# Kernel tuning notes

Measured on AMD Instinct MI355X. Metric: run time of the kernel, lower is better.

The kernel has to match this reference:

```python
import jax, jax.numpy as jnp
import numpy as np

B, H, W, DIM, NH = 4, 32, 32, 768, 12
HD = DIM // NH  # head_dim = 64


def setup_inputs() -> dict:
    key = jax.random.key(0)
    ks = jax.random.split(key, 12)
    n = lambda i, shape, s=1.0: jax.random.normal(ks[i], shape, jnp.float32) * s
    return {
        "q": n(0, (B, H, W, DIM)),
        "k": n(1, (B, H, W, DIM)),
        "v": n(2, (B, H, W, DIM)),
        # Linear weights stored as (in, out) so y = x @ W + b (equivalent to torch x @ W.T)
        "Wq": n(3, (DIM, DIM), 0.02), "bq": jnp.zeros((DIM,), jnp.float32),
        "Wk": n(4, (DIM, DIM), 0.02), "bk": jnp.zeros((DIM,), jnp.float32),
        "Wv": n(5, (DIM, DIM), 0.02), "bv": jnp.zeros((DIM,), jnp.float32),
        "Wp": n(6, (DIM, DIM), 0.02), "bp": jnp.zeros((DIM,), jnp.float32),
        # decomposed relative position tables: (2*size - 1, head_dim)
        "rel_pos_h": n(7, (2 * H - 1, HD), 0.02),
        "rel_pos_w": n(8, (2 * W - 1, HD), 0.02),
    }


def reference(q, k, v, Wq, bq, Wk, bk, Wv, bv, Wp, bp, rel_pos_h, rel_pos_w):
    scale = HD ** -0.5

    def to_heads(x, Wt, b):
        y = x.reshape(B, H * W, DIM) @ Wt + b          # (B, HW, DIM)
        return y.reshape(B, H * W, NH, HD).transpose(0, 2, 1, 3).reshape(B * NH, H * W, HD)

    qh = to_heads(q, Wq, bq)   # (B*NH, HW, HD)
    kh = to_heads(k, Wk, bk)
    vh = to_heads(v, Wv, bv)

    # scaled dot-product scores
    attn = jnp.einsum('bqd,bkd->bqk', qh * scale, kh)  # (B*NH, HW, HW)

    # decomposed relative position bias (q_size == k_size == input_size, no interpolation)
    idx_h = jnp.arange(H)[:, None] - jnp.arange(H)[None, :] + (H - 1)
    idx_w = jnp.arange(W)[:, None] - jnp.arange(W)[None, :] + (W - 1)
    Rh = rel_pos_h[idx_h]  # (H, H, HD)
    Rw = rel_pos_w[idx_w]  # (W, W, HD)
    rq = qh.reshape(B * NH, H, W, HD)  # unscaled q, as in torch add_decomposed_rel_pos
    rel_h = jnp.einsum('bhwc,hkc->bhwk', rq, Rh)  # (B*NH, H, W, H)
    rel_w = jnp.einsum('bhwc,wkc->bhwk', rq, Rw)  # (B*NH, H, W, W)

    attn = (attn.reshape(B * NH, H, W, H, W)
            + rel_h[:, :, :, :, None]
            + rel_w[:, :, :, None, :]).reshape(B * NH, H * W, H * W)

    attn = jax.nn.softmax(attn, axis=-1)
    x = (attn @ vh).reshape(B, NH, H, W, HD).transpose(0, 2, 3, 1, 4).reshape(B, H, W, DIM)
    return x @ Wp + bp
```

## Files before the change

kernel.cpp:

```cpp
#include <hip/hip_runtime.h>
#include <math.h>

#define DIM  768
#define NH   12
#define HD   64
#define HWN  1024
#define MROWS 4096

typedef __attribute__((ext_vector_type(8))) short short8;
typedef __attribute__((ext_vector_type(4))) float f32x4;
typedef _Float16 h8 __attribute__((ext_vector_type(8)));
typedef _Float16 h2 __attribute__((ext_vector_type(2)));

__device__ __forceinline__ void gl_lds16(const void* g, void* l) {
    __builtin_amdgcn_global_load_lds(
        (const __attribute__((address_space(1))) void*)g,
        (__attribute__((address_space(3))) void*)l, 16, 0, 0);
}

__global__ __launch_bounds__(256) void prep_kernel(
    const float* __restrict__ q, const float* __restrict__ k,
    const float* __restrict__ v,
    const float* __restrict__ Wq, const float* __restrict__ Wk,
    const float* __restrict__ Wv, const float* __restrict__ Wp,
    const float* __restrict__ rph, const float* __restrict__ rpw,
    _Float16* __restrict__ WtAll, _Float16* __restrict__ relTg,
    _Float16* __restrict__ xf16)
{
    __shared__ float Ws[64][65];
    const int b = blockIdx.x;
    const int t = threadIdx.x;

    if (b < 576) {
        const int z = b / 144, rem = b - z * 144;
        const int ky = rem / 12, nx = rem - ky * 12;
        const float* W = (z == 0) ? Wq : (z == 1) ? Wk : (z == 2) ? Wv : Wp;
        _Float16* Wt = WtAll + (size_t)z * 589824;
        const int k0 = ky * 64, n0 = nx * 64;
        {
            int r = t >> 2, c4 = (t & 3) * 16;
            #pragma unroll
            for (int u = 0; u < 16; u += 4)
                *(float4*)&Ws[r][c4 + u] = *(const float4*)(W + (size_t)(k0 + r) * DIM + n0 + c4 + u);
        }
        __syncthreads();
        const int n = t >> 2, kseg = (t & 3) * 16;
        h8 h0, h1;
        #pragma unroll
        for (int j = 0; j < 8; ++j) {
            h0[j] = (_Float16)Ws[kseg + j][n];
            h1[j] = (_Float16)Ws[kseg + 8 + j][n];
        }
        size_t base = (size_t)(n0 + n) * DIM + k0 + kseg;
        *(h8*)(Wt + base) = h0;
        *(h8*)(Wt + base + 8) = h1;
    } else if (b == 576) {
        const int row = t >> 1, c0 = (t & 1) * 32;
        const float* src = (row < 63) ? rph + (size_t)row * HD
                         : (row >= 64 && row < 127) ? rpw + (size_t)(row - 64) * HD
                         : nullptr;
        #pragma unroll
        for (int g = 0; g < 4; ++g) {
            h8 o;
            #pragma unroll
            for (int j = 0; j < 8; ++j)
                o[j] = src ? (_Float16)src[c0 + g * 8 + j] : (_Float16)0.0f;
            *(h8*)(relTg + (size_t)row * HD + c0 + g * 8) = o;
        }
    } else {
        const int N8 = MROWS * DIM / 8;
        int i = (b - 577) * 256 + t;
        const int stride = (gridDim.x - 577) * 256;
        for (; i < 3 * N8; i += stride) {
            const int sel = i / N8, j = i - sel * N8;
            const float* src = (sel == 0) ? q : (sel == 1) ? k : v;
            float4 a0 = ((const float4*)src)[j * 2];
            float4 a1 = ((const float4*)src)[j * 2 + 1];
            h8 o = {(_Float16)a0.x, (_Float16)a0.y, (_Float16)a0.z, (_Float16)a0.w,
                    (_Float16)a1.x, (_Float16)a1.y, (_Float16)a1.z, (_Float16)a1.w};
            *(h8*)(xf16 + (size_t)sel * (MROWS * DIM) + (size_t)j * 8) = o;
        }
    }
}

template<int AMODE>
__global__ __launch_bounds__(256, 3) void gemm_mfma_kernel(
    const _Float16* __restrict__ X0, const _Float16* __restrict__ WtAll,
    const float* __restrict__ bias0, const float* __restrict__ bias1,
    const float* __restrict__ bias2,
    void* __restrict__ Y0, void* __restrict__ Y1, void* __restrict__ Y2)
{
    constexpr int MT = (AMODE == 0) ? 128 : 64;
    constexpr int RF = MT / 32;
    __shared__ __align__(16) char smem[MT * 128 + 12 * 1024];
    constexpr int BOFF = MT * 128;

    const int t = threadIdx.x;
    const int w = t >> 6, lane = t & 63;
    const int l15 = lane & 15, l4 = lane >> 4;

    int sel, rb, cb;
    if (AMODE == 0) {
        const int sw = (blockIdx.x & 7) * 96 + (blockIdx.x >> 3);
        sel = sw >> 8;
        const int rem = sw & 255;
        rb = rem >> 3; cb = rem & 7;
    } else {
        const int sw = (blockIdx.x & 7) * 64 + (blockIdx.x >> 3);
        sel = 3;
        rb = sw >> 3; cb = sw & 7;
    }
    const int row0 = rb * MT, col0 = cb * 96;

    const char* Ab = (const char*)(X0 + (AMODE == 0 ? (size_t)sel * (MROWS * DIM) : 0));
    const _Float16* Bt = WtAll + (size_t)sel * 589824;
    const float* bias = (AMODE == 1) ? bias0 : (sel == 0) ? bias0 : (sel == 1) ? bias1 : bias2;

    f32x4 acc[RF][3];
    #pragma unroll
    for (int i = 0; i < RF; ++i)
        #pragma unroll
        for (int j = 0; j < 3; ++j) acc[i][j] = (f32x4){0, 0, 0, 0};

    for (int kt = 0; kt < 12; ++kt) {
        #pragma unroll
        for (int i = 0; i < MT / 32; ++i) {
            const int fi = w * (MT / 32) + i;
            const int row = fi * 8 + (lane >> 3);
            const int srcb = ((lane & 7) * 16) ^ ((row & 7) << 4);
            gl_lds16(Ab + (size_t)(row0 + row) * 1536 + kt * 128 + srcb, smem + fi * 1024);
        }
        #pragma unroll
        for (int it = 0; it < 3; ++it) {
            const int f = it * 4 + w;
            const int ks = f / 6, cf = f % 6;
            const size_t off = (size_t)(col0 + cf * 16 + l15) * 1536 + kt * 128 + ks * 64 + l4 * 16;
            gl_lds16((const char*)Bt + off, smem + BOFF + f * 1024);
        }
        __syncthreads();

        __builtin_amdgcn_s_setprio(1);
        #pragma unroll
        for (int ks = 0; ks < 2; ++ks) {
            h8 b[3];
            #pragma unroll
            for (int cf4 = 0; cf4 < 3; ++cf4) {
                const int fb = ks * 6 + (w & 1) * 3 + cf4;
                b[cf4] = *(const h8*)(smem + BOFF + fb * 1024 + lane * 16);
            }
            #pragma unroll
            for (int rf = 0; rf < RF; ++rf) {
                const int arow = (w >> 1) * (MT / 2) + rf * 16 + l15;
                const int base = arow * 128 + ((ks * 64 + l4 * 16) ^ ((arow & 7) << 4));
                h8 ah = *(const h8*)(smem + base);
                #pragma unroll
                for (int cf4 = 0; cf4 < 3; ++cf4)
                    acc[rf][cf4] = __builtin_amdgcn_mfma_f32_16x16x32_f16(ah, b[cf4], acc[rf][cf4], 0, 0, 0);
            }
        }
        __builtin_amdgcn_s_setprio(0);
        __syncthreads();
    }

    const int wrow0 = row0 + (w >> 1) * (MT / 2);
    const int wcol0 = col0 + (w & 1) * 48;
    #pragma unroll
    for (int cf4 = 0; cf4 < 3; ++cf4) {
        const int c = wcol0 + cf4 * 16 + l15;
        const float bb = bias[c];
        #pragma unroll
        for (int rf = 0; rf < RF; ++rf) {
            #pragma unroll
            for (int reg = 0; reg < 4; ++reg) {
                const int r = wrow0 + rf * 16 + l4 * 4 + reg;
                float y = acc[rf][cf4][reg] + bb;
                if (AMODE == 1) {
                    ((float*)Y0)[(size_t)r * DIM + c] = y;
                } else {
                    _Float16* Yh = (_Float16*)((sel == 0) ? Y0 : (sel == 1) ? Y1 : Y2);
                    size_t base = ((size_t)((r >> 10) * NH + (c >> 6)) * HWN + (r & 1023)) * HD + (c & 63);
                    Yh[base] = (_Float16)y;
                }
            }
        }
    }
}

#define AT_REL   0
#define AT_VT    8704
#define AT_P     25088
#define AT_KB    33280
#define AT_QF    8704
#define AT_RELT  17920
#define AT_PG    17920
#define AT_OF    8704
#define AT_TOTAL 49664

__global__ __launch_bounds__(256, 3) void attn_kernel(
    const _Float16* __restrict__ qh, const _Float16* __restrict__ kh,
    const _Float16* __restrict__ vh, const _Float16* __restrict__ relTg,
    _Float16* __restrict__ aout)
{
    __shared__ __align__(16) char smem[AT_TOTAL];
    const int bid = blockIdx.x;
    const int j   = bid >> 3;
    const int bh  = (bid & 7) * 6 + (j >> 4);
    const int qb  = j & 15;
    const int t  = threadIdx.x;
    const int w  = t >> 6;
    const int lane = t & 63;
    const int l15 = lane & 15, l4 = lane >> 4;

    _Float16* Rel = (_Float16*)(smem + AT_REL);
    _Float16* Qf  = (_Float16*)(smem + AT_QF);

    const int r = t >> 2, dc = (t & 3) * 16;
    {
        const _Float16* qp = qh + ((size_t)bh * HWN + qb * 64 + r) * HD + dc;
        *(short8*)(&Qf[r * 72 + dc])     = *(const short8*)(qp);
        *(short8*)(&Qf[r * 72 + dc + 8]) = *(const short8*)(qp + 8);
        #pragma unroll
        for (int it = 0; it < 4; ++it) {
            const int f = it * 4 + w;
            const int ct = f >> 1, ks = f & 1;
            gl_lds16((const char*)relTg + (ct * 16 + l15) * 128 + ks * 64 + l4 * 16,
                     smem + AT_RELT + f * 1024);
        }
    }
    __syncthreads();

    const _Float16* kb_ = kh + (size_t)bh * HWN * HD;
    const _Float16* vb_ = vh + (size_t)bh * HWN * HD;
    const int key2 = (t & 31) * 2, dgrp = t >> 5;
    short8 rv0, rv1;
#define LOADV(KT) {                                                            \
        const _Float16* vp = vb_ + (size_t)((KT) * 64 + key2) * HD + dgrp * 8; \
        rv0 = *(const short8*)vp; rv1 = *(const short8*)(vp + HD); }
    LOADV(0);

    h8 qf2[2];
    {
        const int qr = w * 16 + l15;
        qf2[0] = *(const h8*)(&Qf[qr * 72 + l4 * 8]);
        qf2[1] = *(const h8*)(&Qf[qr * 72 + 32 + l4 * 8]);
        #pragma unroll
        for (int j2 = 0; j2 < 8; ++j2) { qf2[0][j2] *= (_Float16)0.125f; qf2[1][j2] *= (_Float16)0.125f; }
    }

    f32x4 pacc[4][2];
    #pragma unroll
    for (int i = 0; i < 4; ++i)
        #pragma unroll
        for (int j2 = 0; j2 < 2; ++j2) pacc[i][j2] = (f32x4){0, 0, 0, 0};
    #pragma unroll
    for (int ks = 0; ks < 2; ++ks) {
        h8 b0 = *(const h8*)(smem + AT_RELT + ((w * 2 + 0) * 2 + ks) * 1024 + lane * 16);
        h8 b1 = *(const h8*)(smem + AT_RELT + ((w * 2 + 1) * 2 + ks) * 1024 + lane * 16);
        #pragma unroll
        for (int rt = 0; rt < 4; ++rt) {
            h8 a = *(const h8*)(&Qf[(rt * 16 + l15) * 72 + ks * 32 + l4 * 8]);
            pacc[rt][0] = __builtin_amdgcn_mfma_f32_16x16x32_f16(a, b0, pacc[rt][0], 0, 0, 0);
            pacc[rt][1] = __builtin_amdgcn_mfma_f32_16x16x32_f16(a, b1, pacc[rt][1], 0, 0, 0);
        }
    }

    __syncthreads();
    _Float16* Pg = (_Float16*)(smem + AT_PG);
    #pragma unroll
    for (int rt = 0; rt < 4; ++rt)
        #pragma unroll
        for (int cb2 = 0; cb2 < 2; ++cb2)
            #pragma unroll
            for (int reg = 0; reg < 4; ++reg)
                Pg[(rt * 16 + l4 * 4 + reg) * 130 + w * 32 + cb2 * 16 + l15] =
                    (_Float16)pacc[rt][cb2][reg];
    __syncthreads();

    {
        const int q = t >> 2, kk0 = (t & 3) * 8;
        const int hw = qb * 64 + q;
        const int hq = hw >> 5, wq = hw & 31;
        short8 vh_, vw_;
        #pragma unroll
        for (int j2 = 0; j2 < 8; ++j2) {
            const int kk = kk0 + j2;
            vh_[j2] = *(const short*)&Pg[q * 130 + (hq + 31 - kk)];
            vw_[j2] = *(const short*)&Pg[q * 130 + 64 + (wq + 31 - kk)];
        }
        *(short8*)(&Rel[q * 68 + kk0])      = vh_;
        *(short8*)(&Rel[q * 68 + 32 + kk0]) = vw_;
    }
    __syncthreads();

    const int qrow_bias = w * 16 + l15;
    float rw_[2][4];
    #pragma unroll
    for (int c2 = 0; c2 < 2; ++c2)
        #pragma unroll
        for (int reg = 0; reg < 4; ++reg)
            rw_[c2][reg] = (float)Rel[qrow_bias * 68 + 32 + c2 * 16 + l4 * 4 + reg];

#define STAGEK(KT, BUF) {                                                      \
        _Pragma("unroll")                                                      \
        for (int i2 = 0; i2 < 2; ++i2) {                                       \
            const int f = w * 2 + i2;                                          \
            const int keyk = f * 8 + (lane >> 3);                              \
            const int srcb = ((lane & 7) * 16) ^ ((lane >> 3) << 4);           \
            gl_lds16((const char*)kb_ + (size_t)((KT) * 64 + keyk) * 128 + srcb, \
                     smem + AT_KB + (BUF) * 8192 + f * 1024);                  \
        } }

#define WRITEVT(BUF) {                                                         \
        _Pragma("unroll")                                                      \
        for (int j2 = 0; j2 < 8; ++j2) {                                       \
            const int d = dgrp * 8 + j2;                                       \
            unsigned pk = ((unsigned short)rv0[j2]) |                          \
                          (((unsigned)(unsigned short)rv1[j2]) << 16);         \
            *(unsigned*)(smem + AT_VT + (BUF) * 8192 + d * 128 +               \
                         ((key2 * 2) ^ ((d & 7) << 4))) = pk; } }
    WRITEVT(0);
    STAGEK(0, 0);

    f32x4 acc_o[4] = {{0,0,0,0},{0,0,0,0},{0,0,0,0},{0,0,0,0}};
    float m_ = -INFINITY, lsum = 0.f;
    char* Pw = smem + AT_P + w * 2048;
    const int swzP = (l15 & 7) << 4;

    #pragma unroll 2
    for (int kt = 0; kt < 16; ++kt) {
        const int cur = kt & 1;
        __syncthreads();
        if (kt < 15) { LOADV(kt + 1); STAGEK(kt + 1, cur ^ 1); }

        h2 rhp = *(const h2*)(&Rel[qrow_bias * 68 + kt * 2]);
        const float rh0 = (float)rhp[0];
        const float rh1 = (float)rhp[1];
        f32x4 accs[4];
        #pragma unroll
        for (int ct = 0; ct < 4; ++ct) {
            const float rhc = (ct >> 1) ? rh1 : rh0;
            #pragma unroll
            for (int reg = 0; reg < 4; ++reg)
                accs[ct][reg] = rw_[ct & 1][reg] + rhc;
        }
        __builtin_amdgcn_s_setprio(1);
        #pragma unroll
        for (int ct = 0; ct < 4; ++ct) {
            const int row = ct * 16 + l15;
            const int swzK = (row & 7) << 4;
            #pragma unroll
            for (int ks = 0; ks < 2; ++ks) {
                h8 kfr = *(const h8*)(smem + AT_KB + cur * 8192 + row * 128 +
                                      ((ks * 64 + l4 * 16) ^ swzK));
                accs[ct] = __builtin_amdgcn_mfma_f32_16x16x32_f16(kfr, qf2[ks], accs[ct], 0, 0, 0);
            }
        }
        __builtin_amdgcn_s_setprio(0);

        float mx[4];
        #pragma unroll
        for (int ct = 0; ct < 4; ++ct)
            mx[ct] = fmaxf(fmaxf(accs[ct][0], accs[ct][1]),
                           fmaxf(accs[ct][2], accs[ct][3]));
        float tmax = fmaxf(fmaxf(mx[0], mx[1]), fmaxf(mx[2], mx[3]));

        if (__any(tmax > m_ + 8.f)) {
            float tg = fmaxf(tmax, __shfl_xor(tmax, 16));
            tg = fmaxf(tg, __shfl_xor(tg, 32));
            const float mnew = fmaxf(m_, tg);
            const float factor = __expf(m_ - mnew);
            m_ = mnew;
            lsum *= factor;
            #pragma unroll
            for (int reg = 0; reg < 4; ++reg) {
                const float fr = __shfl(factor, l4 * 4 + reg);
                #pragma unroll
                for (int dt = 0; dt < 4; ++dt) acc_o[dt][reg] *= fr;
            }
        }

        float tsum = 0.f;
        #pragma unroll
        for (int ct = 0; ct < 4; ++ct) {
            float p0 = __expf(accs[ct][0] - m_);
            float p1 = __expf(accs[ct][1] - m_);
            float p2 = __expf(accs[ct][2] - m_);
            float p3 = __expf(accs[ct][3] - m_);
            tsum += (p0 + p1) + (p2 + p3);
            h2 pa = {(_Float16)p0, (_Float16)p1};
            h2 pb = {(_Float16)p2, (_Float16)p3};
            uint2 pk;
            pk.x = *(unsigned*)&pa;
            pk.y = *(unsigned*)&pb;
            *(uint2*)(Pw + l15 * 128 + ((ct * 32 + l4 * 8) ^ swzP)) = pk;
        }
        lsum += tsum;

        __builtin_amdgcn_s_setprio(1);
        #pragma unroll
        for (int ks = 0; ks < 2; ++ks) {
            h8 pa = *(const h8*)(Pw + l15 * 128 + ((ks * 64 + l4 * 16) ^ swzP));
            #pragma unroll
            for (int dt = 0; dt < 4; ++dt) {
                const int d = dt * 16 + l15;
                h8 vf = *(const h8*)(smem + AT_VT + cur * 8192 + d * 128 +
                                     ((ks * 64 + l4 * 16) ^ ((d & 7) << 4)));
                acc_o[dt] = __builtin_amdgcn_mfma_f32_16x16x32_f16(pa, vf, acc_o[dt], 0, 0, 0);
            }
        }
        __builtin_amdgcn_s_setprio(0);

        if (kt < 15) WRITEVT(cur ^ 1);
    }

    float ltot = lsum + __shfl_xor(lsum, 16);
    ltot += __shfl_xor(ltot, 32);
    const float invl = 1.0f / ltot;
    float linv[4];
    #pragma unroll
    for (int reg = 0; reg < 4; ++reg) linv[reg] = __shfl(invl, l4 * 4 + reg);
    __syncthreads();
    _Float16* Of = (_Float16*)(smem + AT_OF);
    #pragma unroll
    for (int reg = 0; reg < 4; ++reg) {
        const int qloc = w * 16 + l4 * 4 + reg;
        #pragma unroll
        for (int dt = 0; dt < 4; ++dt)
            Of[qloc * 72 + dt * 16 + l15] = (_Float16)(acc_o[dt][reg] * linv[reg]);
    }
    __syncthreads();
    {
        const int b_ = bh / NH, nh = bh % NH;
        _Float16* op = aout + ((size_t)b_ * HWN + qb * 64 + r) * DIM + nh * HD + dc;
        *(short8*)op       = *(const short8*)(&Of[r * 72 + dc]);
        *(short8*)(op + 8) = *(const short8*)(&Of[r * 72 + dc + 8]);
    }
}

extern "C" void kernel_launch(void* const* d_in, const int* in_sizes, int n_in,
                              void* d_out, int out_size, void* d_ws, size_t ws_size,
                              hipStream_t stream) {
    const float* q   = (const float*)d_in[0];
    const float* k   = (const float*)d_in[1];
    const float* v   = (const float*)d_in[2];
    const float* Wq  = (const float*)d_in[3];
    const float* bq  = (const float*)d_in[4];
    const float* Wk  = (const float*)d_in[5];
    const float* bk  = (const float*)d_in[6];
    const float* Wv  = (const float*)d_in[7];
    const float* bv  = (const float*)d_in[8];
    const float* Wp  = (const float*)d_in[9];
    const float* bp  = (const float*)d_in[10];
    const float* rph = (const float*)d_in[11];
    const float* rpw = (const float*)d_in[12];

    float* out = (float*)d_out;
    char*  w0  = (char*)d_ws;

    _Float16* wtAll = (_Float16*)(w0);
    _Float16* relTg = (_Float16*)(w0 + 4718592);
    _Float16* xf16  = (_Float16*)(w0 + 4734976);
    _Float16* aout  = (_Float16*)(w0 + 4734976);
    _Float16* qf16  = (_Float16*)(w0 + 23609344);
    _Float16* kf16  = (_Float16*)(w0 + 29900800);
    _Float16* vf16  = (_Float16*)(w0 + 36192256);

    dim3 blk(256);
    prep_kernel<<<2625, blk, 0, stream>>>(q, k, v, Wq, Wk, Wv, Wp, rph, rpw,
                                          wtAll, relTg, xf16);
    gemm_mfma_kernel<0><<<768, blk, 0, stream>>>(
        xf16, wtAll, bq, bk, bv, qf16, kf16, vf16);
    attn_kernel<<<768, blk, 0, stream>>>(qf16, kf16, vf16, relTg, aout);
    gemm_mfma_kernel<1><<<512, blk, 0, stream>>>(
        aout, wtAll, bp, nullptr, nullptr, out, nullptr, nullptr);
}
```

Measured before the change: 91.17 us.

## Double-buffer GEMM LDS tiles with halved K-step to overlap loads and MFMA

The projection GEMM's main loop now stages tiles into two LDS buffers, with K-tiles halved from 64 to 32 halves (24 iterations instead of 12). The next tile's global-to-LDS loads are issued right after the barrier, before the current tile's MFMAs, and one of the two barriers per iteration is dropped. The aim is to hide global load latency behind compute. The trade-off is more iterations, each doing less MFMA work per barrier, and a changed LDS swizzle pattern.

```diff
diff --git a/kernel.cpp b/kernel.cpp
--- a/kernel.cpp
+++ b/kernel.cpp
@@ -92,8 +92,10 @@
 {
     constexpr int MT = (AMODE == 0) ? 128 : 64;
     constexpr int RF = MT / 32;
-    __shared__ __align__(16) char smem[MT * 128 + 12 * 1024];
-    constexpr int BOFF = MT * 128;
+    constexpr int ABYTES = MT * 64;
+    constexpr int BUFB   = ABYTES + 6144;
+    constexpr int NAOPS  = MT / 16;
+    __shared__ __align__(16) char smem[2 * BUFB];
 
     const int t = threadIdx.x;
     const int w = t >> 6, lane = t & 63;
@@ -122,44 +124,44 @@
         #pragma unroll
         for (int j = 0; j < 3; ++j) acc[i][j] = (f32x4){0, 0, 0, 0};
 
-    for (int kt = 0; kt < 12; ++kt) {
-        #pragma unroll
-        for (int i = 0; i < MT / 32; ++i) {
-            const int fi = w * (MT / 32) + i;
-            const int row = fi * 8 + (lane >> 3);
-            const int srcb = ((lane & 7) * 16) ^ ((row & 7) << 4);
-            gl_lds16(Ab + (size_t)(row0 + row) * 1536 + kt * 128 + srcb, smem + fi * 1024);
-        }
-        #pragma unroll
-        for (int it = 0; it < 3; ++it) {
-            const int f = it * 4 + w;
-            const int ks = f / 6, cf = f % 6;
-            const size_t off = (size_t)(col0 + cf * 16 + l15) * 1536 + kt * 128 + ks * 64 + l4 * 16;
-            gl_lds16((const char*)Bt + off, smem + BOFF + f * 1024);
-        }
+#define GSTAGE(KT, BUF) {                                                      \
+        char* dst = smem + (BUF) * BUFB;                                       \
+        _Pragma("unroll")                                                      \
+        for (int op = w; op < NAOPS + 6; op += 4) {                            \
+            if (op < NAOPS) {                                                  \
+                const int row = op * 16 + (lane >> 2);                         \
+                const int srcb = ((lane & 3) * 16) ^ ((row & 3) << 4);         \
+                gl_lds16(Ab + (size_t)(row0 + row) * 1536 + (KT) * 64 + srcb,  \
+                         dst + op * 1024);                                     \
+            } else {                                                           \
+                const int cf = op - NAOPS;                                     \
+                gl_lds16((const char*)Bt + (size_t)(col0 + cf * 16 + l15) * 1536 \
+                         + (KT) * 64 + l4 * 16, dst + ABYTES + cf * 1024);     \
+            }                                                                  \
+        } }
+
+    GSTAGE(0, 0);
+
+    #pragma unroll 2
+    for (int kt = 0; kt < 24; ++kt) {
         __syncthreads();
+        if (kt < 23) GSTAGE(kt + 1, (kt + 1) & 1);
+        const char* buf = smem + (kt & 1) * BUFB;
 
         __builtin_amdgcn_s_setprio(1);
-        #pragma unroll
-        for (int ks = 0; ks < 2; ++ks) {
-            h8 b[3];
-            #pragma unroll
-            for (int cf4 = 0; cf4 < 3; ++cf4) {
-                const int fb = ks * 6 + (w & 1) * 3 + cf4;
-                b[cf4] = *(const h8*)(smem + BOFF + fb * 1024 + lane * 16);
-            }
-            #pragma unroll
-            for (int rf = 0; rf < RF; ++rf) {
-                const int arow = (w >> 1) * (MT / 2) + rf * 16 + l15;
-                const int base = arow * 128 + ((ks * 64 + l4 * 16) ^ ((arow & 7) << 4));
-                h8 ah = *(const h8*)(smem + base);
-                #pragma unroll
-                for (int cf4 = 0; cf4 < 3; ++cf4)
-                    acc[rf][cf4] = __builtin_amdgcn_mfma_f32_16x16x32_f16(ah, b[cf4], acc[rf][cf4], 0, 0, 0);
-            }
+        h8 b[3];
+        #pragma unroll
+        for (int cf4 = 0; cf4 < 3; ++cf4)
+            b[cf4] = *(const h8*)(buf + ABYTES + ((w & 1) * 3 + cf4) * 1024 + lane * 16);
+        #pragma unroll
+        for (int rf = 0; rf < RF; ++rf) {
+            const int arow = (w >> 1) * (MT / 2) + rf * 16 + l15;
+            h8 ah = *(const h8*)(buf + arow * 64 + ((l4 * 16) ^ ((arow & 3) << 4)));
+            #pragma unroll
+            for (int cf4 = 0; cf4 < 3; ++cf4)
+                acc[rf][cf4] = __builtin_amdgcn_mfma_f32_16x16x32_f16(ah, b[cf4], acc[rf][cf4], 0, 0, 0);
         }
         __builtin_amdgcn_s_setprio(0);
-        __syncthreads();
     }
 
     const int wrow0 = row0 + (w >> 1) * (MT / 2);
```

Measured after the change: 91.87 us. No clear change (+0.8%).
